# Optimization experiments

Measured on AMD Instinct MI355X. Metric: run time of the kernel, lower is better.

Reference implementation:

```python
import jax, jax.numpy as jnp
import numpy as np

N_NODES = 50000


def gcn_conv(x, src, dst, norm, W, b):
    # x: [N, Fin] -> linear transform then normalized scatter-add aggregation
    h = x @ W  # [N, Fout]
    msg = h[src] * norm[:, None]  # [E', Fout] gather + scale
    out = jax.ops.segment_sum(msg, dst, num_segments=N_NODES)  # scatter-add
    return out + b


def _build_graph(edge_index):
    # add self-loops (PyG GCNConv default) and compute symmetric normalization
    n = N_NODES
    loops = jnp.arange(n, dtype=edge_index.dtype)
    src = jnp.concatenate([edge_index[0], loops])
    dst = jnp.concatenate([edge_index[1], loops])
    deg = jax.ops.segment_sum(jnp.ones_like(dst, dtype=jnp.float32), dst, num_segments=n)
    dinv = jnp.where(deg > 0, jax.lax.rsqrt(deg), 0.0)
    norm = dinv[src] * dinv[dst]  # [E+N]
    return src, dst, norm


def setup_inputs() -> dict:
    key = jax.random.key(0)
    ks = jax.random.split(key, 8)
    in_c, out_c = 128, 64
    hid = 2 * out_c
    n_edges = 800000
    x = jax.random.normal(ks[0], (N_NODES, in_c), dtype=jnp.float32)
    edge_index = jax.random.randint(ks[1], (2, n_edges), 0, N_NODES, dtype=jnp.int64)
    s = 1.0 / np.sqrt(in_c)
    W1 = jax.random.uniform(ks[2], (in_c, hid), minval=-s, maxval=s, dtype=jnp.float32)
    b1 = jnp.zeros((hid,), dtype=jnp.float32)
    s2 = 1.0 / np.sqrt(hid)
    W_mu = jax.random.uniform(ks[3], (hid, out_c), minval=-s2, maxval=s2, dtype=jnp.float32)
    b_mu = jnp.zeros((out_c,), dtype=jnp.float32)
    W_ls = jax.random.uniform(ks[4], (hid, out_c), minval=-s2, maxval=s2, dtype=jnp.float32)
    b_ls = jnp.zeros((out_c,), dtype=jnp.float32)
    return {"x": x, "edge_index": edge_index, "W1": W1, "b1": b1,
            "W_mu": W_mu, "b_mu": b_mu, "W_ls": W_ls, "b_ls": b_ls}


def reference(x, edge_index, W1, b1, W_mu, b_mu, W_ls, b_ls):
    src, dst, norm = _build_graph(edge_index)
    h = jax.nn.relu(gcn_conv(x, src, dst, norm, W1, b1))
    mu = gcn_conv(h, src, dst, norm, W_mu, b_mu)
    logstd = gcn_conv(h, src, dst, norm, W_ls, b_ls)
    return mu, logstd
```

## Files before the change

### kernel.cpp

```cpp
#include <hip/hip_runtime.h>

#define N_NODES 50000
#define NE      800000
#define FDIM    128
#define OUTC    64
#define CAP     64
#define NXCD    8
#define SLICE   6250
#define NCHK    391

typedef _Float16 half4 __attribute__((ext_vector_type(4)));
typedef _Float16 f16x8 __attribute__((ext_vector_type(8)));
typedef float    f32x4 __attribute__((ext_vector_type(4)));



__global__ __launch_bounds__(256) void k_prep(int4* __restrict__ deg4,
                                              const float* __restrict__ W1,
                                              const float* __restrict__ Wmu,
                                              const float* __restrict__ Wls,
                                              const float* __restrict__ bmu,
                                              const float* __restrict__ bls,
                                              _Float16* __restrict__ W1T,
                                              _Float16* __restrict__ WoT,
                                              float* __restrict__ bo) {
    int b = blockIdx.x, tid = threadIdx.x;
    if (b < 49) {
        int i = b * 256 + tid;
        if (i < 12500) deg4[i] = make_int4(0, 0, 0, 0);
    } else {
        int j = (b - 49) * 256 + tid;
        if (j < 16384) {
            int n = j >> 7, k = j & 127;
            W1T[j] = (_Float16)W1[k * 128 + n];
        } else if (j < 32768) {
            int jj = j - 16384;
            int n = jj >> 7, k = jj & 127;
            WoT[jj] = (_Float16)(n < 64 ? Wmu[k * 64 + n] : Wls[k * 64 + (n - 64)]);
        } else if (j < 32896) {
            int n = j - 32768;
            bo[n] = (n < 64) ? bmu[n] : bls[n - 64];
        }
    }
}


__global__ __launch_bounds__(256) void k_count_fill(const int* __restrict__ ei,
                                                    int* __restrict__ deg,
                                                    int* __restrict__ pks) {
    int bid = blockIdx.x;
    int k8  = bid & 7;
    int lo  = k8 * SLICE;
    int chunk = bid >> 3;
    int base = chunk * 2048 + threadIdx.x;
    #pragma unroll
    for (int j = 0; j < 8; ++j) {
        int e = base + j * 256;
        if (e < NE) {
            int d = ei[NE + e];
            unsigned int rel = (unsigned int)(d - lo);
            if (rel < SLICE) {
                int s = ei[e];
                int slot = atomicAdd(&deg[d], 1);
                if (slot < CAP) pks[d * CAP + slot] = s;
            }
        }
    }
}


__global__ __launch_bounds__(256) void k_scale(const float* __restrict__ x,
                                               const int* __restrict__ deg,
                                               float* __restrict__ dinv,
                                               _Float16* __restrict__ x16) {
    int i = blockIdx.x * 256 + threadIdx.x;
    if (i >= (N_NODES * FDIM) / 4) return;
    int node = i >> 5;
    float dv = rsqrtf((float)(deg[node] + 1));
    if ((i & 31) == 0) dinv[node] = dv;
    float4 v = reinterpret_cast<const float4*>(x)[i];
    half4 h = {(_Float16)(dv * v.x), (_Float16)(dv * v.y),
               (_Float16)(dv * v.z), (_Float16)(dv * v.w)};
    reinterpret_cast<half4*>(x16)[i] = h;
}


__device__ __forceinline__ void add8h(float* a, f16x8 h) {
    #pragma unroll
    for (int j = 0; j < 8; ++j) a[j] += (float)h[j];
}

__device__ __forceinline__ void agg_tile(const _Float16* __restrict__ in,
                                         const int* __restrict__ pks,
                                         const int* __restrict__ deg,
                                         const float* __restrict__ dinv,
                                         _Float16 (*__restrict__ As)[136]) {
    int tid = threadIdx.x;
    int rl = tid >> 4;
    int r  = blockIdx.x * 16 + rl;
    int lane8 = (tid & 15) * 8;
    int cnt = deg[r]; if (cnt > CAP) cnt = CAP;
    const int* prow = pks + r * CAP;
    float a0[8] = {0,0,0,0,0,0,0,0};
    float a1[8] = {0,0,0,0,0,0,0,0};
    int e = 0;
    for (; e + 4 <= cnt; e += 4) {
        int s0 = prow[e], s1 = prow[e+1], s2 = prow[e+2], s3 = prow[e+3];
        f16x8 x0 = *reinterpret_cast<const f16x8*>(&in[(size_t)s0 * FDIM + lane8]);
        f16x8 x1 = *reinterpret_cast<const f16x8*>(&in[(size_t)s1 * FDIM + lane8]);
        f16x8 x2 = *reinterpret_cast<const f16x8*>(&in[(size_t)s2 * FDIM + lane8]);
        f16x8 x3 = *reinterpret_cast<const f16x8*>(&in[(size_t)s3 * FDIM + lane8]);
        add8h(a0, x0); add8h(a1, x1); add8h(a0, x2); add8h(a1, x3);
    }
    for (; e < cnt; ++e)
        add8h(a0, *reinterpret_cast<const f16x8*>(&in[(size_t)prow[e] * FDIM + lane8]));
    add8h(a1, *reinterpret_cast<const f16x8*>(&in[(size_t)r * FDIM + lane8]));
    float dv = dinv[r];
    f16x8 g;
    #pragma unroll
    for (int j = 0; j < 8; ++j) g[j] = (_Float16)(dv * (a0[j] + a1[j]));
    *reinterpret_cast<f16x8*>(&As[rl][lane8]) = g;
}


__global__ __launch_bounds__(256) void k_layer1(const _Float16* __restrict__ x16,
                                                const int* __restrict__ pks,
                                                const int* __restrict__ deg,
                                                const float* __restrict__ dinv,
                                                const _Float16* __restrict__ W1T,
                                                const float* __restrict__ b1,
                                                _Float16* __restrict__ H16) {
    __shared__ _Float16 As[16][136];
    agg_tile(x16, pks, deg, dinv, As);
    __syncthreads();
    int tid = threadIdx.x;
    int wave = tid >> 6, lane = tid & 63;
    int colg = lane & 15;
    int kg8 = (lane >> 4) * 8;
    f32x4 acc0 = {0.f, 0.f, 0.f, 0.f}, acc1 = {0.f, 0.f, 0.f, 0.f};
    #pragma unroll
    for (int ks = 0; ks < 4; ++ks) {
        f16x8 a  = *reinterpret_cast<const f16x8*>(&As[colg][ks * 32 + kg8]);
        f16x8 b0 = *reinterpret_cast<const f16x8*>(
            &W1T[(size_t)((2 * wave) * 16 + colg) * FDIM + ks * 32 + kg8]);
        f16x8 b1v = *reinterpret_cast<const f16x8*>(
            &W1T[(size_t)((2 * wave + 1) * 16 + colg) * FDIM + ks * 32 + kg8]);
        acc0 = __builtin_amdgcn_mfma_f32_16x16x32_f16(a, b0, acc0, 0, 0, 0);
        acc1 = __builtin_amdgcn_mfma_f32_16x16x32_f16(a, b1v, acc1, 0, 0, 0);
    }
    int r0 = (lane >> 4) * 4;
    #pragma unroll
    for (int t = 0; t < 2; ++t) {
        int col = (2 * wave + t) * 16 + colg;
        float bias = b1[col];
        f32x4 acc = t ? acc1 : acc0;
        #pragma unroll
        for (int r = 0; r < 4; ++r) {
            int m = blockIdx.x * 16 + r0 + r;
            float h = fmaxf(acc[r] + bias, 0.f);
            H16[(size_t)m * FDIM + col] = (_Float16)(dinv[m] * h);
        }
    }
}

__global__ __launch_bounds__(256) void k_layer2(const _Float16* __restrict__ h16,
                                                const int* __restrict__ pks,
                                                const int* __restrict__ deg,
                                                const float* __restrict__ dinv,
                                                const _Float16* __restrict__ WoT,
                                                const float* __restrict__ bo,
                                                float* __restrict__ MU,
                                                float* __restrict__ LS) {
    __shared__ _Float16 As[16][136];
    agg_tile(h16, pks, deg, dinv, As);
    __syncthreads();
    int tid = threadIdx.x;
    int wave = tid >> 6, lane = tid & 63;
    int colg = lane & 15;
    int kg8 = (lane >> 4) * 8;
    f32x4 acc0 = {0.f, 0.f, 0.f, 0.f}, acc1 = {0.f, 0.f, 0.f, 0.f};
    #pragma unroll
    for (int ks = 0; ks < 4; ++ks) {
        f16x8 a  = *reinterpret_cast<const f16x8*>(&As[colg][ks * 32 + kg8]);
        f16x8 b0 = *reinterpret_cast<const f16x8*>(
            &WoT[(size_t)((2 * wave) * 16 + colg) * FDIM + ks * 32 + kg8]);
        f16x8 b1v = *reinterpret_cast<const f16x8*>(
            &WoT[(size_t)((2 * wave + 1) * 16 + colg) * FDIM + ks * 32 + kg8]);
        acc0 = __builtin_amdgcn_mfma_f32_16x16x32_f16(a, b0, acc0, 0, 0, 0);
        acc1 = __builtin_amdgcn_mfma_f32_16x16x32_f16(a, b1v, acc1, 0, 0, 0);
    }
    int r0 = (lane >> 4) * 4;
    #pragma unroll
    for (int t = 0; t < 2; ++t) {
        int col = (2 * wave + t) * 16 + colg;
        float bias = bo[col];
        f32x4 acc = t ? acc1 : acc0;
        #pragma unroll
        for (int r = 0; r < 4; ++r) {
            int m = blockIdx.x * 16 + r0 + r;
            float v = acc[r] + bias;
            if (col < 64) MU[(size_t)m * OUTC + col] = v;
            else          LS[(size_t)m * OUTC + (col - 64)] = v;
        }
    }
}


extern "C" void kernel_launch(void* const* d_in, const int* in_sizes, int n_in,
                              void* d_out, int out_size, void* d_ws, size_t ws_size,
                              hipStream_t stream) {
    const float* x   = (const float*)d_in[0];
    const int*   ei  = (const int*)d_in[1];
    const float* W1  = (const float*)d_in[2];
    const float* b1  = (const float*)d_in[3];
    const float* Wmu = (const float*)d_in[4];
    const float* bmu = (const float*)d_in[5];
    const float* Wls = (const float*)d_in[6];
    const float* bls = (const float*)d_in[7];
    float* out = (float*)d_out;

    char* ws = (char*)d_ws;
    int*      deg  = (int*)     (ws + 0);
    float*    dinv = (float*)   (ws + 200000);
    int*      pks  = (int*)     (ws + 400000);
    _Float16* W1T  = (_Float16*)(ws + 13200000);
    _Float16* WoT  = (_Float16*)(ws + 13232768);
    float*    bo   = (float*)   (ws + 13265536);
    _Float16* h16  = (_Float16*)(ws + 13266048);

    _Float16* x16 = (_Float16*)d_out;

    k_prep      <<<49 + 129, 256, 0, stream>>>((int4*)deg, W1, Wmu, Wls, bmu, bls,
                                               W1T, WoT, bo);
    k_count_fill<<<NXCD * NCHK, 256, 0, stream>>>(ei, deg, pks);
    k_scale     <<<(N_NODES * FDIM / 4 + 255) / 256, 256, 0, stream>>>(x, deg, dinv, x16);

    k_layer1<<<N_NODES / 16, 256, 0, stream>>>(x16, pks, deg, dinv, W1T, b1, h16);
    k_layer2<<<N_NODES / 16, 256, 0, stream>>>(h16, pks, deg, dinv, WoT, bo,
                                               out, out + (size_t)N_NODES * OUTC);
}
```

Baseline: 142.5 us.

## Sort nodes by degree via counting-sort permutation to balance aggregation work

Adds a histogram kernel and a counting-sort permutation kernel that order nodes by in-degree, capped at 63. Both layer kernels then process rows in permuted order, so each 16-row tile holds nodes of similar degree and the 16-thread groups in a block finish together. The cost is two extra small kernel launches, an indirection load per row, and output stores scattered across rows instead of contiguous. It also zeroes the histogram counters in the prep kernel.

```diff
diff --git a/kernel.cpp b/kernel.cpp
--- a/kernel.cpp
+++ b/kernel.cpp
@@ -16,6 +16,7 @@
 
 
 __global__ __launch_bounds__(256) void k_prep(int4* __restrict__ deg4,
+                                              int4* __restrict__ hz,
                                               const float* __restrict__ W1,
                                               const float* __restrict__ Wmu,
                                               const float* __restrict__ Wls,
@@ -28,8 +29,10 @@
     if (b < 49) {
         int i = b * 256 + tid;
         if (i < 12500) deg4[i] = make_int4(0, 0, 0, 0);
+    } else if (b == 49) {
+        if (tid < 32) hz[tid] = make_int4(0, 0, 0, 0);
     } else {
-        int j = (b - 49) * 256 + tid;
+        int j = (b - 50) * 256 + tid;
         if (j < 16384) {
             int n = j >> 7, k = j & 127;
             W1T[j] = (_Float16)W1[k * 128 + n];
@@ -85,6 +88,54 @@
 }
 
 
+__global__ __launch_bounds__(256) void k_hist(const int* __restrict__ deg,
+                                              int* __restrict__ gHist) {
+    __shared__ int lh[64];
+    int tid = threadIdx.x;
+    if (tid < 64) lh[tid] = 0;
+    __syncthreads();
+    int r = blockIdx.x * 256 + tid;
+    if (r < N_NODES) {
+        int d = deg[r]; if (d > 63) d = 63;
+        atomicAdd(&lh[d], 1);
+    }
+    __syncthreads();
+    if (tid < 64 && lh[tid] > 0) atomicAdd(&gHist[tid], lh[tid]);
+}
+
+__global__ __launch_bounds__(256) void k_perm(const int* __restrict__ deg,
+                                              const int* __restrict__ gHist,
+                                              int* __restrict__ gCur,
+                                              int* __restrict__ perm) {
+    __shared__ int lh[64], cb[64], bb[64];
+    int tid = threadIdx.x;
+    if (tid < 64) lh[tid] = 0;
+    __syncthreads();
+    int r = blockIdx.x * 256 + tid;
+    int d = 0, rank = 0;
+    bool valid = (r < N_NODES);
+    if (valid) {
+        d = deg[r]; if (d > 63) d = 63;
+        rank = atomicAdd(&lh[d], 1);
+    }
+    __syncthreads();
+    if (tid < 64) {
+        int c = lh[tid];
+        cb[tid] = (c > 0) ? atomicAdd(&gCur[tid], c) : 0;
+        int v = gHist[tid];
+        int sc = v;
+        #pragma unroll
+        for (int off = 1; off < 64; off <<= 1) {
+            int t = __shfl_up(sc, off);
+            if (tid >= off) sc += t;
+        }
+        bb[tid] = sc - v;
+    }
+    __syncthreads();
+    if (valid) perm[bb[d] + cb[d] + rank] = r;
+}
+
+
 __device__ __forceinline__ void add8h(float* a, f16x8 h) {
     #pragma unroll
     for (int j = 0; j < 8; ++j) a[j] += (float)h[j];
@@ -94,10 +145,11 @@
                                          const int* __restrict__ pks,
                                          const int* __restrict__ deg,
                                          const float* __restrict__ dinv,
+                                         const int* __restrict__ perm,
                                          _Float16 (*__restrict__ As)[136]) {
     int tid = threadIdx.x;
     int rl = tid >> 4;
-    int r  = blockIdx.x * 16 + rl;
+    int r  = perm[blockIdx.x * 16 + rl];
     int lane8 = (tid & 15) * 8;
     int cnt = deg[r]; if (cnt > CAP) cnt = CAP;
     const int* prow = pks + r * CAP;
@@ -127,11 +179,12 @@
                                                 const int* __restrict__ pks,
                                                 const int* __restrict__ deg,
                                                 const float* __restrict__ dinv,
+                                                const int* __restrict__ perm,
                                                 const _Float16* __restrict__ W1T,
                                                 const float* __restrict__ b1,
                                                 _Float16* __restrict__ H16) {
     __shared__ _Float16 As[16][136];
-    agg_tile(x16, pks, deg, dinv, As);
+    agg_tile(x16, pks, deg, dinv, perm, As);
     __syncthreads();
     int tid = threadIdx.x;
     int wave = tid >> 6, lane = tid & 63;
@@ -149,16 +202,19 @@
         acc1 = __builtin_amdgcn_mfma_f32_16x16x32_f16(a, b1v, acc1, 0, 0, 0);
     }
     int r0 = (lane >> 4) * 4;
+    int mbase = blockIdx.x * 16 + r0;
+    int mp[4]; float dvm[4];
+    #pragma unroll
+    for (int rg = 0; rg < 4; ++rg) { mp[rg] = perm[mbase + rg]; dvm[rg] = dinv[mp[rg]]; }
     #pragma unroll
     for (int t = 0; t < 2; ++t) {
         int col = (2 * wave + t) * 16 + colg;
         float bias = b1[col];
         f32x4 acc = t ? acc1 : acc0;
         #pragma unroll
-        for (int r = 0; r < 4; ++r) {
-            int m = blockIdx.x * 16 + r0 + r;
-            float h = fmaxf(acc[r] + bias, 0.f);
-            H16[(size_t)m * FDIM + col] = (_Float16)(dinv[m] * h);
+        for (int rg = 0; rg < 4; ++rg) {
+            float h = fmaxf(acc[rg] + bias, 0.f);
+            H16[(size_t)mp[rg] * FDIM + col] = (_Float16)(dvm[rg] * h);
         }
     }
 }
@@ -167,12 +223,13 @@
                                                 const int* __restrict__ pks,
                                                 const int* __restrict__ deg,
                                                 const float* __restrict__ dinv,
+                                                const int* __restrict__ perm,
                                                 const _Float16* __restrict__ WoT,
                                                 const float* __restrict__ bo,
                                                 float* __restrict__ MU,
                                                 float* __restrict__ LS) {
     __shared__ _Float16 As[16][136];
-    agg_tile(h16, pks, deg, dinv, As);
+    agg_tile(h16, pks, deg, dinv, perm, As);
     __syncthreads();
     int tid = threadIdx.x;
     int wave = tid >> 6, lane = tid & 63;
@@ -190,17 +247,20 @@
         acc1 = __builtin_amdgcn_mfma_f32_16x16x32_f16(a, b1v, acc1, 0, 0, 0);
     }
     int r0 = (lane >> 4) * 4;
+    int mbase = blockIdx.x * 16 + r0;
+    int mp[4];
+    #pragma unroll
+    for (int rg = 0; rg < 4; ++rg) mp[rg] = perm[mbase + rg];
     #pragma unroll
     for (int t = 0; t < 2; ++t) {
         int col = (2 * wave + t) * 16 + colg;
         float bias = bo[col];
         f32x4 acc = t ? acc1 : acc0;
         #pragma unroll
-        for (int r = 0; r < 4; ++r) {
-            int m = blockIdx.x * 16 + r0 + r;
-            float v = acc[r] + bias;
-            if (col < 64) MU[(size_t)m * OUTC + col] = v;
-            else          LS[(size_t)m * OUTC + (col - 64)] = v;
+        for (int rg = 0; rg < 4; ++rg) {
+            float v = acc[rg] + bias;
+            if (col < 64) MU[(size_t)mp[rg] * OUTC + col] = v;
+            else          LS[(size_t)mp[rg] * OUTC + (col - 64)] = v;
         }
     }
 }
@@ -220,22 +280,27 @@
     float* out = (float*)d_out;
 
     char* ws = (char*)d_ws;
-    int*      deg  = (int*)     (ws + 0);
-    float*    dinv = (float*)   (ws + 200000);
-    int*      pks  = (int*)     (ws + 400000);
-    _Float16* W1T  = (_Float16*)(ws + 13200000);
-    _Float16* WoT  = (_Float16*)(ws + 13232768);
-    float*    bo   = (float*)   (ws + 13265536);
-    _Float16* h16  = (_Float16*)(ws + 13266048);
+    int*      deg   = (int*)     (ws + 0);
+    float*    dinv  = (float*)   (ws + 200000);
+    int*      pks   = (int*)     (ws + 400000);
+    _Float16* W1T   = (_Float16*)(ws + 13200000);
+    _Float16* WoT   = (_Float16*)(ws + 13232768);
+    float*    bo    = (float*)   (ws + 13265536);
+    int*      gHist = (int*)     (ws + 13266048);
+    int*      gCur  = (int*)     (ws + 13266304);
+    int*      perm  = (int*)     (ws + 13266560);
+    _Float16* h16   = (_Float16*)(ws + 13466560);
 
     _Float16* x16 = (_Float16*)d_out;
 
-    k_prep      <<<49 + 129, 256, 0, stream>>>((int4*)deg, W1, Wmu, Wls, bmu, bls,
-                                               W1T, WoT, bo);
+    k_prep      <<<50 + 129, 256, 0, stream>>>((int4*)deg, (int4*)gHist,
+                                               W1, Wmu, Wls, bmu, bls, W1T, WoT, bo);
     k_count_fill<<<NXCD * NCHK, 256, 0, stream>>>(ei, deg, pks);
     k_scale     <<<(N_NODES * FDIM / 4 + 255) / 256, 256, 0, stream>>>(x, deg, dinv, x16);
-
-    k_layer1<<<N_NODES / 16, 256, 0, stream>>>(x16, pks, deg, dinv, W1T, b1, h16);
-    k_layer2<<<N_NODES / 16, 256, 0, stream>>>(h16, pks, deg, dinv, WoT, bo,
+    k_hist      <<<(N_NODES + 255) / 256, 256, 0, stream>>>(deg, gHist);
+    k_perm      <<<(N_NODES + 255) / 256, 256, 0, stream>>>(deg, gHist, gCur, perm);
+
+    k_layer1<<<N_NODES / 16, 256, 0, stream>>>(x16, pks, deg, dinv, perm, W1T, b1, h16);
+    k_layer2<<<N_NODES / 16, 256, 0, stream>>>(h16, pks, deg, dinv, perm, WoT, bo,
                                                out, out + (size_t)N_NODES * OUTC);
 }
```

New measurement: 151.4 us. 6.2% more time.
